# Performance work log

Measured on AMD Instinct MI355X. Metric: run time of the kernel, lower is better.

Reference implementation:

```python
import jax, jax.numpy as jnp
import numpy as np

F = 128; K = 64; SR_CUT = 10.0
NB = 5; NRI = 3; NRA = 2; NRO = 1
N_ATOMS = 10000; N_PAIRS = 320000


def act(x):
    # shifted softplus: softplus(x) - log(2)
    return jax.nn.softplus(x) - jnp.log(2.0).astype(x.dtype)


def residual(x, W1, b1, W2, b2):
    # PhysNet residual: x + dense2(dense1(act(x))) with activation on dense1
    h = act(act(x) @ W1 + b1)
    return x + h @ W2 + b2


def cutoff_fn(D):
    x = D / SR_CUT
    x3 = x * x * x; x4 = x3 * x; x5 = x4 * x
    return jnp.where(x < 1.0, 1.0 - 6.0 * x5 + 15.0 * x4 - 10.0 * x3, 0.0)


def setup_inputs() -> dict:
    key = jax.random.key(0)
    ks = jax.random.split(key, 24)

    def nrm(k, shape, s=0.05):
        return (jax.random.normal(k, shape) * s).astype(jnp.float32)

    inp = {}
    inp["Z"] = jax.random.randint(ks[0], (N_ATOMS,), 1, 95)
    inp["R"] = (jax.random.normal(ks[1], (N_ATOMS, 3)) * 3.0).astype(jnp.float32)
    inp["idx_i"] = jax.random.randint(ks[2], (N_PAIRS,), 0, N_ATOMS)
    inp["idx_j"] = jax.random.randint(ks[3], (N_PAIRS,), 0, N_ATOMS)
    s3 = float(np.sqrt(3.0))
    inp["embeddings"] = jax.random.uniform(ks[4], (95, F), minval=-s3, maxval=s3).astype(jnp.float32)
    inp["rbf_centers"] = jnp.linspace(1.0, float(np.exp(-SR_CUT)), K).astype(jnp.float32)
    width = (0.5 / ((1.0 - float(np.exp(-SR_CUT))) / K)) ** 2
    inp["rbf_widths"] = jnp.full((K,), width, dtype=jnp.float32)
    inp["k2f_W"] = nrm(ks[5], (NB, K, F))
    inp["Wi"] = nrm(ks[6], (NB, F, F)); inp["bi"] = jnp.zeros((NB, F), jnp.float32)
    inp["Wj"] = nrm(ks[7], (NB, F, F)); inp["bj"] = jnp.zeros((NB, F), jnp.float32)
    inp["ri_W1"] = nrm(ks[8], (NB, NRI, F, F)); inp["ri_b1"] = jnp.zeros((NB, NRI, F), jnp.float32)
    inp["ri_W2"] = nrm(ks[9], (NB, NRI, F, F)); inp["ri_b2"] = jnp.zeros((NB, NRI, F), jnp.float32)
    inp["dW"] = nrm(ks[10], (NB, F, F)); inp["db"] = jnp.zeros((NB, F), jnp.float32)
    inp["u"] = jnp.ones((NB, F), jnp.float32)
    inp["ra_W1"] = nrm(ks[11], (NB, NRA, F, F)); inp["ra_b1"] = jnp.zeros((NB, NRA, F), jnp.float32)
    inp["ra_W2"] = nrm(ks[12], (NB, NRA, F, F)); inp["ra_b2"] = jnp.zeros((NB, NRA, F), jnp.float32)
    inp["ro_W1"] = nrm(ks[13], (NB, NRO, F, F)); inp["ro_b1"] = jnp.zeros((NB, NRO, F), jnp.float32)
    inp["ro_W2"] = nrm(ks[14], (NB, NRO, F, F)); inp["ro_b2"] = jnp.zeros((NB, NRO, F), jnp.float32)
    inp["out_W"] = nrm(ks[15], (NB, F, 2))
    inp["Escale"] = jnp.ones((95,), jnp.float32); inp["Eshift"] = jnp.zeros((95,), jnp.float32)
    inp["Qscale"] = jnp.ones((95,), jnp.float32); inp["Qshift"] = jnp.zeros((95,), jnp.float32)
    return inp


def reference(Z, R, idx_i, idx_j, embeddings, rbf_centers, rbf_widths, k2f_W, Wi, bi, Wj, bj,
              ri_W1, ri_b1, ri_W2, ri_b2, dW, db, u, ra_W1, ra_b1, ra_W2, ra_b2,
              ro_W1, ro_b1, ro_W2, ro_b2, out_W, Escale, Eshift, Qscale, Qshift):
    N = R.shape[0]
    # gather-based interatomic distances: gather -> sub -> sumsq -> relu -> sqrt
    dR = R[idx_i] - R[idx_j]                                   # [P,3]
    Dij = jnp.sqrt(jax.nn.relu(jnp.sum(dR * dR, axis=-1)))     # [P]
    # RBF expansion with smooth cutoff
    rbf = cutoff_fn(Dij)[:, None] * jnp.exp(-rbf_widths * (jnp.exp(-Dij)[:, None] - rbf_centers) ** 2)  # [P,K]
    x = embeddings[Z]                                          # [N,F]
    Ea = jnp.zeros((N,), x.dtype)
    Qa = jnp.zeros((N,), x.dtype)
    nhloss = jnp.zeros((), x.dtype)
    last2 = None
    for b in range(NB):
        # --- interaction layer ---
        g = rbf @ k2f_W[b]                                     # [P,F]
        xa = act(x)
        xi = act(xa @ Wi[b] + bi[b])                           # [N,F]
        xj_feat = act(xa @ Wj[b] + bj[b])                      # [N,F]
        msg = g * xj_feat[idx_j]                               # [P,F] gather + modulate
        m = xi + jax.ops.segment_sum(msg, idx_i, num_segments=N)
        for l in range(NRI):
            m = residual(m, ri_W1[b, l], ri_b1[b, l], ri_W2[b, l], ri_b2[b, l])
        m = act(m)
        x = u[b] * x + m @ dW[b] + db[b]
        for l in range(NRA):
            x = residual(x, ra_W1[b, l], ra_b1[b, l], ra_W2[b, l], ra_b2[b, l])
        # --- output block ---
        o = x
        for l in range(NRO):
            o = residual(o, ro_W1[b, l], ro_b1[b, l], ro_W2[b, l], ro_b2[b, l])
        out = act(o) @ out_W[b]                                # [N,2] -> (Ea, Qa)
        Ea = Ea + out[:, 0]
        Qa = Qa + out[:, 1]
        out2 = out * out
        if b > 0:
            nhloss = nhloss + jnp.mean(out2 / (out2 + last2 + 1e-7))
        last2 = out2
    Ea = Escale[Z] * Ea + Eshift[Z]
    Qa = Qscale[Z] * Qa + Qshift[Z]
    return Ea, Qa, Dij, nhloss
```

## Files before the change

### kernel.cpp

```cpp
#include <hip/hip_runtime.h>

typedef __attribute__((ext_vector_type(8))) short bfrag;
typedef __attribute__((ext_vector_type(4))) float ffrag;

__device__ __forceinline__ unsigned short f2b(float f){
  unsigned int u = __float_as_uint(f);
  return (unsigned short)((u + 0x7FFFu + ((u >> 16) & 1u)) >> 16);
}
__device__ __forceinline__ float b2f_lo(unsigned int v){
  return __uint_as_float(v << 16);
}
__device__ __forceinline__ float b2f_hi(unsigned int v){
  return __uint_as_float(v & 0xFFFF0000u);
}
__device__ __forceinline__ float actf(float v){
  float e = __builtin_amdgcn_exp2f(-fabsf(v)*1.44269504088896341f);
  return fmaxf(v, 0.f) + __builtin_amdgcn_logf(1.f + e)*0.69314718055994531f - 0.69314718055994531f;
}

__global__ __launch_bounds__(256) void k_zero(float* p, int n){
  int i = blockIdx.x*256 + threadIdx.x;
  if (i < n) p[i] = 0.f;
}

__global__ __launch_bounds__(256) void k_dij_count(
    const float* __restrict__ R, const int* __restrict__ idx_i, const int* __restrict__ idx_j,
    float* __restrict__ DijF, float* __restrict__ Dout, int* __restrict__ counts, int P){
  int p = blockIdx.x*256 + threadIdx.x;
  if (p >= P) return;
  int i = idx_i[p], j = idx_j[p];
  float dx = R[i*3+0] - R[j*3+0];
  float dy = R[i*3+1] - R[j*3+1];
  float dz = R[i*3+2] - R[j*3+2];
  float D = sqrtf(fmaxf(dx*dx + dy*dy + dz*dz, 0.f));
  DijF[p] = D;
  Dout[p] = D;
  atomicAdd(&counts[i], 1);
}

__global__ __launch_bounds__(1024) void k_scan(const int* __restrict__ counts,
    int* __restrict__ cursor, int N){
  __shared__ int wsum[16];
  int tid = threadIdx.x;
  int CH = (N + 1023) >> 10;
  int base = tid * CH;
  int s = 0;
  for (int i = 0; i < CH; ++i){
    int idx = base + i;
    s += (idx < N) ? counts[idx] : 0;
  }
  int lane = tid & 63, w = tid >> 6;
  int v = s;
  #pragma unroll
  for (int off = 1; off < 64; off <<= 1){
    int t = __shfl_up(v, off, 64);
    if (lane >= off) v += t;
  }
  if (lane == 63) wsum[w] = v;
  __syncthreads();
  if (tid < 16){
    int t = wsum[tid];
    int vv = t;
    #pragma unroll
    for (int off = 1; off < 16; off <<= 1){
      int u = __shfl_up(vv, off, 64);
      if (tid >= off) vv += u;
    }
    wsum[tid] = vv - t;
  }
  __syncthreads();
  int run = (v - s) + wsum[w];
  for (int i = 0; i < CH; ++i){
    int idx = base + i;
    if (idx < N){ cursor[idx] = run; run += counts[idx]; }
  }
}

__global__ __launch_bounds__(256) void k_scatter(const int* __restrict__ idx_i,
    const int* __restrict__ idx_j, const float* __restrict__ DijF,
    int* __restrict__ cursor, int* __restrict__ i_s, int* __restrict__ j_s,
    float* __restrict__ D_s, int P){
  int p = blockIdx.x*256 + threadIdx.x;
  if (p >= P) return;
  int i = idx_i[p];
  int pos = atomicAdd(&cursor[i], 1);
  i_s[pos] = i;
  j_s[pos] = idx_j[p];
  D_s[pos] = DijF[p];
}

__global__ __launch_bounds__(256) void k_rbf(
    const float* __restrict__ D_s, const float* __restrict__ cent, const float* __restrict__ wid,
    unsigned short* __restrict__ rbf_s, int P){
  int gid = blockIdx.x*256 + threadIdx.x;
  if (gid >= P*8) return;
  int t = gid >> 3, kg = gid & 7;
  float D = D_s[t];
  float xc = D * 0.1f;
  float cut = 0.f;
  if (xc < 1.f){
    float x3 = xc*xc*xc, x4 = x3*xc, x5 = x4*xc;
    cut = 1.f - 6.f*x5 + 15.f*x4 - 10.f*x3;
  }
  float eD = __builtin_amdgcn_exp2f(-D*1.44269504088896341f);
  bfrag o;
  #pragma unroll
  for (int i = 0; i < 8; ++i){
    int k = kg*8 + i;
    float tt = eD - cent[k];
    float v = cut * __builtin_amdgcn_exp2f(-wid[k]*tt*tt*1.44269504088896341f);
    o[i] = (short)f2b(v);
  }
  *(bfrag*)(rbf_s + (size_t)gid*8) = o;
}

__global__ __launch_bounds__(256) void k_prepAll(
    const float* __restrict__ riW1, const float* __restrict__ riW2,
    const float* __restrict__ dW,   const float* __restrict__ raW1,
    const float* __restrict__ raW2, const float* __restrict__ roW1,
    const float* __restrict__ roW2, const float* __restrict__ Wi,
    const float* __restrict__ Wj,   const float* __restrict__ k2f,
    const float* __restrict__ outW,
    unsigned short* __restrict__ WBall, unsigned short* __restrict__ k2fP,
    unsigned short* __restrict__ outWB){
  int gid = blockIdx.x*256 + threadIdx.x;
  if (gid < 75*2048){
    int i = gid >> 11, r = gid & 2047;
    const float* S;
    int slot;
    if (i < 15)      { S = riW1 + (size_t)i*16384;      slot = (i/3)*15 + 2*(i%3); }
    else if (i < 30) { int j=i-15; S = riW2 + (size_t)j*16384; slot = (j/3)*15 + 2*(j%3) + 1; }
    else if (i < 35) { int j=i-30; S = dW   + (size_t)j*16384; slot = j*15 + 6; }
    else if (i < 45) { int j=i-35; S = raW1 + (size_t)j*16384; slot = (j/2)*15 + 7 + 2*(j%2); }
    else if (i < 55) { int j=i-45; S = raW2 + (size_t)j*16384; slot = (j/2)*15 + 8 + 2*(j%2); }
    else if (i < 60) { int j=i-55; S = roW1 + (size_t)j*16384; slot = j*15 + 11; }
    else if (i < 65) { int j=i-60; S = roW2 + (size_t)j*16384; slot = j*15 + 12; }
    else if (i < 70) { int j=i-65; S = Wi   + (size_t)j*16384; slot = ((j==0)?4:(j-1))*15 + 13; }
    else             { int j=i-70; S = Wj   + (size_t)j*16384; slot = ((j==0)?4:(j-1))*15 + 14; }
    int fr = r >> 6, l = r & 63;
    int T = fr >> 2, k0 = fr & 3;
    int n = T*16 + (l & 15);
    int kbase = k0*32 + (l >> 4)*8;
    unsigned short* D = WBall + ((size_t)slot*2048 + r)*8;
    ushort4 o0, o1;
    o0.x=f2b(S[(kbase+0)*128+n]); o0.y=f2b(S[(kbase+1)*128+n]);
    o0.z=f2b(S[(kbase+2)*128+n]); o0.w=f2b(S[(kbase+3)*128+n]);
    o1.x=f2b(S[(kbase+4)*128+n]); o1.y=f2b(S[(kbase+5)*128+n]);
    o1.z=f2b(S[(kbase+6)*128+n]); o1.w=f2b(S[(kbase+7)*128+n]);
    ((ushort4*)D)[0]=o0; ((ushort4*)D)[1]=o1;
  } else if (gid < 75*2048 + 5120){
    int g = gid - 75*2048;
    int l = g & 63, fr = (g >> 6) & 15, b = g >> 10;
    int tile = fr >> 1, kh = fr & 1;
    const float* src = k2f + (size_t)b*64*128;
    int n = tile*16 + (l & 15);
    int kbase = kh*32 + (l >> 4)*8;
    ushort4 o0, o1;
    o0.x = f2b(src[(kbase+0)*128+n]); o0.y = f2b(src[(kbase+1)*128+n]);
    o0.z = f2b(src[(kbase+2)*128+n]); o0.w = f2b(src[(kbase+3)*128+n]);
    o1.x = f2b(src[(kbase+4)*128+n]); o1.y = f2b(src[(kbase+5)*128+n]);
    o1.z = f2b(src[(kbase+6)*128+n]); o1.w = f2b(src[(kbase+7)*128+n]);
    ushort4* dst = (ushort4*)(k2fP + (size_t)g*8);
    dst[0] = o0; dst[1] = o1;
  } else if (gid < 75*2048 + 5120 + 1280){
    int g = gid - (75*2048 + 5120);
    int b = g >> 8, r = g & 255;
// ... 24 lines not shown
  #pragma unroll
  for (int tt = 0; tt < 4; ++tt){
    ffrag c = {0.f,0.f,0.f,0.f};
    const bfrag* bp = (const bfrag*)(WB + (((w*4+tt)*4)*64 + l)*8);
    #pragma unroll
    for (int k0 = 0; k0 < 4; ++k0)
      c = __builtin_amdgcn_mfma_f32_16x16x32_bf16(A[k0], bp[k0*64], c, 0, 0, 0);
    C[tt] = c;
  }
}

__global__ __launch_bounds__(128) void k_phase1m(
    const int* __restrict__ Z, const float* __restrict__ emb,
    const unsigned short* __restrict__ WB45,
    const float* __restrict__ bi0, const float* __restrict__ bj0,
    float* __restrict__ x_g, float* __restrict__ m_g, unsigned short* __restrict__ xjb_g, int N){
  __shared__ unsigned short tile[16*136];
  int tid = threadIdx.x, w = tid >> 6, l = tid & 63;
  int m = l & 15, q = l >> 4, rbase = blockIdx.x*16;
  #pragma unroll
  for (int r = 0; r < 4; ++r){
    int row = rbase + q*4 + r;
    int z = Z[row];
    #pragma unroll
    for (int tt = 0; tt < 4; ++tt){
      int c = (w*4+tt)*16 + m;
      float v = emb[(size_t)z*128 + c];
      x_g[(size_t)row*128 + c] = v;
      tile[(q*4+r)*136 + c] = f2b(actf(v));
    }
  }
  __syncthreads();
  ffrag C[4];
  mmtile(tile, WB45 + 13*16384, w, l, C);
  #pragma unroll
  for (int tt = 0; tt < 4; ++tt){
    int c = (w*4+tt)*16 + m;
    float bb = bi0[c];
    #pragma unroll
    for (int r = 0; r < 4; ++r)
      m_g[(size_t)(rbase + q*4 + r)*128 + c] = actf(C[tt][r] + bb);
  }
  mmtile(tile, WB45 + 14*16384, w, l, C);
  #pragma unroll
  for (int tt = 0; tt < 4; ++tt){
    int c = (w*4+tt)*16 + m;
    float bb = bj0[c];
    #pragma unroll
    for (int r = 0; r < 4; ++r)
      xjb_g[(size_t)(rbase + q*4 + r)*128 + c] = f2b(actf(C[tt][r] + bb));
  }
}

__global__ __launch_bounds__(256) void k_pairmsg2(
    const unsigned short* __restrict__ rbf_s, const unsigned short* __restrict__ k2fP,
    const int* __restrict__ i_s, const int* __restrict__ j_s,
    const unsigned short* __restrict__ xj, float* __restrict__ m_g, int P){
  __shared__ float G[4][16*130];
  int tid = threadIdx.x, w = tid >> 6, l = tid & 63;
  float* Gw = &G[w][0];
  bfrag B[16];
  #pragma unroll
  for (int t = 0; t < 8; ++t){
    #pragma unroll
    for (int kh = 0; kh < 2; ++kh)
      B[t*2+kh] = *(const bfrag*)(k2fP + (size_t)((t*2+kh)*64 + l)*8);
  }
  int wstart = (blockIdx.x*4 + w)*128;
  if (wstart >= P) return;
  int row16 = l & 15, quad = l >> 4;
  float a0 = 0.f, a1 = 0.f;
  int iCur = -1;
  bfrag A0 = *(const bfrag*)(rbf_s + (size_t)(wstart + row16)*64 + quad*8);
  bfrag A1 = *(const bfrag*)(rbf_s + (size_t)(wstart + row16)*64 + 32 + quad*8);
  int4 iv[4], jv[4];
  #pragma unroll
  for (int g = 0; g < 4; ++g){
    iv[g] = *(const int4*)(i_s + wstart + g*4);
    jv[g] = *(const int4*)(j_s + wstart + g*4);
  }
  unsigned int xv[16];
  {
    const int* jp = (const int*)jv;
    #pragma unroll
    for (int k = 0; k < 16; ++k)
      xv[k] = *(const unsigned int*)(xj + (size_t)jp[k]*128 + 2*l);
  }
  #pragma unroll 1
  for (int bi2 = 0; bi2 < 8; ++bi2){
    int bt = wstart + bi2*16;
    const int* ip = (const int*)iv;
    int4 niv[4], njv[4];
    if (bi2 < 7){
      int btn = bt + 16;
      #pragma unroll
      for (int g = 0; g < 4; ++g){
        niv[g] = *(const int4*)(i_s + btn + g*4);
        njv[g] = *(const int4*)(j_s + btn + g*4);
      }
    }
    #pragma unroll
    for (int t = 0; t < 8; ++t){
      ffrag C = {0.f,0.f,0.f,0.f};
      C = __builtin_amdgcn_mfma_f32_16x16x32_bf16(A0, B[t*2],   C, 0, 0, 0);
      C = __builtin_amdgcn_mfma_f32_16x16x32_bf16(A1, B[t*2+1], C, 0, 0, 0);
      #pragma unroll
      for (int r = 0; r < 4; ++r)
        Gw[(quad*4+r)*130 + t*16 + row16] = C[r];
    }
    bfrag nA0, nA1;
    unsigned int nxv[16];
    if (bi2 < 7){
      int btn = bt + 16;
      nA0 = *(const bfrag*)(rbf_s + (size_t)(btn + row16)*64 + quad*8);
      nA1 = *(const bfrag*)(rbf_s + (size_t)(btn + row16)*64 + 32 + quad*8);
      const int* njp = (const int*)njv;
      #pragma unroll
      for (int k = 0; k < 16; ++k)
        nxv[k] = *(const unsigned int*)(xj + (size_t)njp[k]*128 + 2*l);
    }
    #pragma unroll
    for (int k = 0; k < 16; ++k){
      int i = ip[k];
      if (i != iCur){
        if (iCur >= 0){
          unsafeAtomicAdd(&m_g[(size_t)iCur*128 + 2*l],     a0);
          unsafeAtomicAdd(&m_g[(size_t)iCur*128 + 2*l + 1], a1);
        }
        iCur = i; a0 = 0.f; a1 = 0.f;
      }
      float g0 = Gw[k*130 + 2*l], g1 = Gw[k*130 + 2*l + 1];
      a0 = fmaf(g0, b2f_lo(xv[k]), a0);
      a1 = fmaf(g1, b2f_hi(xv[k]), a1);
    }
    if (bi2 < 7){
      A0 = nA0; A1 = nA1;
      #pragma unroll
      for (int g = 0; g < 4; ++g){ iv[g] = niv[g]; jv[g] = njv[g]; }
      #pragma unroll
      for (int k = 0; k < 16; ++k) xv[k] = nxv[k];
    }
  }
  if (iCur >= 0){
    unsafeAtomicAdd(&m_g[(size_t)iCur*128 + 2*l],     a0);
    unsafeAtomicAdd(&m_g[(size_t)iCur*128 + 2*l + 1], a1);
  }
}

template<int HASNEXT, int NH>
__global__ __launch_bounds__(512) void k_phase2m(
    float* __restrict__ m_g, float* __restrict__ x_g, unsigned short* __restrict__ xjb_g,
    const unsigned short* __restrict__ WBb,
    const float* __restrict__ rib1, const float* __restrict__ rib2,
    const float* __restrict__ db, const float* __restrict__ u,
    const float* __restrict__ rab1, const float* __restrict__ rab2,
    const float* __restrict__ rob1, const float* __restrict__ rob2,
    const float* __restrict__ biN, const float* __restrict__ bjN,
    const unsigned short* __restrict__ outWBb,
    float* __restrict__ Ea, float* __restrict__ Qa,
    float* __restrict__ last2, float* __restrict__ nh, int N){
  __shared__ unsigned short tiles[2][2][16*136];
  __shared__ float biasS[16*128];
  int tid = threadIdx.x, w = tid >> 6, l = tid & 63;
  int m = l & 15, q = l >> 4, rbase = blockIdx.x*32;
  int c = w*16 + m;
  ffrag mC[2], xC[2], C[2];
  float xrow[2][4];
  int cur = 0;
  const int nst = HASNEXT ? 15 : 13;
  const int slotSeq[15] = {0,1,2,3,4,5,6,7,8,9,10,
                           HASNEXT?13:11, HASNEXT?14:12, 11, 12};
  bfrag Bb[2][4];
  #pragma unroll
  for (int k0 = 0; k0 < 4; ++k0)
    Bb[0][k0] = *(const bfrag*)(WBb + (size_t)slotSeq[0]*16384 + (size_t)((w*4+k0)*64 + l)*8);

  if (tid < 128){
    biasS[0*128+tid]  = rib1[tid];
    biasS[1*128+tid]  = rib1[128+tid];
    biasS[2*128+tid]  = rib1[256+tid];
    biasS[3*128+tid]  = rib2[tid];
    biasS[4*128+tid]  = rib2[128+tid];
    biasS[5*128+tid]  = rib2[256+tid];
    biasS[6*128+tid]  = db[tid];
    biasS[7*128+tid]  = u[tid];
    biasS[8*128+tid]  = rab1[tid];
    biasS[9*128+tid]  = rab1[128+tid];
    biasS[10*128+tid] = rab2[tid];
    biasS[11*128+tid] = rab2[128+tid];
    biasS[12*128+tid] = rob1[tid];
    biasS[13*128+tid] = rob2[tid];
    biasS[14*128+tid] = biN[tid];
    biasS[15*128+tid] = bjN[tid];
  }
  #pragma unroll
  for (int h = 0; h < 2; ++h){
    #pragma unroll
    for (int r = 0; r < 4; ++r){
      int row = rbase + h*16 + q*4 + r;
      int rs = row < N ? row : N-1;
      xrow[h][r] = x_g[(size_t)rs*128 + c];
      float v = m_g[(size_t)rs*128 + c];
      mC[h][r] = v;
      tiles[h][0][(q*4+r)*136 + c] = f2b(actf(v));
    }
  }
  #pragma unroll 2
  for (int s = 0; s < nst; ++s){
    __syncthreads();
    if (s+1 < nst){
      #pragma unroll
      for (int k0 = 0; k0 < 4; ++k0)
        Bb[(s+1)&1][k0] = *(const bfrag*)(WBb + (size_t)slotSeq[s+1]*16384 + (size_t)((w*4+k0)*64 + l)*8);
    }
    #pragma unroll
    for (int h = 0; h < 2; ++h){
      const unsigned short* tp = &tiles[h][cur][0];
      ffrag cc = {0.f,0.f,0.f,0.f};
      #pragma unroll
      for (int k0 = 0; k0 < 4; ++k0){
        bfrag A = *(const bfrag*)(tp + m*136 + k0*32 + q*8);
        cc = __builtin_amdgcn_mfma_f32_16x16x32_bf16(A, Bb[s&1][k0], cc, 0, 0, 0);
      }
      C[h] = cc;
    }
    if (HASNEXT && s == 11){
      float bb = biasS[14*128 + c];
      #pragma unroll
      for (int h = 0; h < 2; ++h)
        #pragma unroll
        for (int r = 0; r < 4; ++r){
          int row = rbase + h*16 + q*4 + r;
          if (row < N) m_g[(size_t)row*128 + c] = actf(C[h][r] + bb);
        }
    } else if (HASNEXT && s == 12){
      float bb = biasS[15*128 + c];
      #pragma unroll
      for (int h = 0; h < 2; ++h)
        #pragma unroll
        for (int r = 0; r < 4; ++r){
          int row = rbase + h*16 + q*4 + r;
          if (row < N) xjb_g[(size_t)row*128 + c] = f2b(actf(C[h][r] + bb));
        }
    } else if (s == 6){
      float uu = biasS[7*128 + c], bb = biasS[6*128 + c];
      #pragma unroll
      for (int h = 0; h < 2; ++h)
        #pragma unroll
        for (int r = 0; r < 4; ++r){
          float nv = uu*xrow[h][r] + C[h][r] + bb;
          xC[h][r] = nv;
          tiles[h][1-cur][(q*4+r)*136 + c] = f2b(actf(nv));
        }
      cur ^= 1;
    } else if (s == 1 || s == 3 || s == 5){
      float bb = biasS[(3 + (s>>1))*128 + c];
      #pragma unroll
      for (int h = 0; h < 2; ++h)
        #pragma unroll
        for (int r = 0; r < 4; ++r){
          float nv = mC[h][r] + C[h][r] + bb;
          mC[h][r] = nv;
          tiles[h][1-cur][(q*4+r)*136 + c] = f2b(actf(nv));
        }
      cur ^= 1;
    } else if (s == 8 || s == 10){
      float bb = biasS[(10 + ((s-8)>>1))*128 + c];
      #pragma unroll
      for (int h = 0; h < 2; ++h)
        #pragma unroll
        for (int r = 0; r < 4; ++r){
          float nv = xC[h][r] + C[h][r] + bb;
          xC[h][r] = nv;
          tiles[h][1-cur][(q*4+r)*136 + c] = f2b(actf(nv));
          if (HASNEXT && s == 10){
            int row = rbase + h*16 + q*4 + r;
            if (row < N) x_g[(size_t)row*128 + c] = nv;
          }
        }
      cur ^= 1;
    } else if ((HASNEXT && s == 14) || (!HASNEXT && s == 12)){
      float bb = biasS[13*128 + c];
      #pragma unroll
      for (int h = 0; h < 2; ++h)
        #pragma unroll
        for (int r = 0; r < 4; ++r){
          float ov = xC[h][r] + C[h][r] + bb;
          tiles[h][1-cur][(q*4+r)*136 + c] = f2b(actf(ov));
        }
      cur ^= 1;
    } else {
      int bidx = (s==0)?0:(s==2)?1:(s==4)?2:(s==7)?8:(s==9)?9:12;
      float bb = biasS[bidx*128 + c];
      #pragma unroll
      for (int h = 0; h < 2; ++h)
        #pragma unroll
        for (int r = 0; r < 4; ++r)
          tiles[h][1-cur][(q*4+r)*136 + c] = f2b(actf(C[h][r] + bb));
      cur ^= 1;
    }
  }
  __syncthreads();
  if (w < 2){
    const unsigned short* tp = &tiles[w][cur][0];
    bfrag A[4];
    #pragma unroll
    for (int k0 = 0; k0 < 4; ++k0)
      A[k0] = *(const bfrag*)(tp + m*136 + k0*32 + q*8);
    ffrag Ch = {0.f,0.f,0.f,0.f};
    #pragma unroll
    for (int k0 = 0; k0 < 4; ++k0){
      bfrag B = *(const bfrag*)(outWBb + (size_t)(k0*64 + l)*8);
      Ch = __builtin_amdgcn_mfma_f32_16x16x32_bf16(A[k0], B, Ch, 0, 0, 0);
    }
    int col = m;
    if (col < 2){
      float tpa = 0.f;
      #pragma unroll
      for (int r = 0; r < 4; ++r){
        int row = rbase + w*16 + q*4 + r;
        if (row < N){
          float val = Ch[r];
          if (NH){
            if (col == 0) Ea[row] += val; else Qa[row] += val;
          } else {
            if (col == 0) Ea[row]  = val; else Qa[row]  = val;
          }
          float sq = val*val;
          if (NH){
            float lastv = last2[row*2 + col];
            tpa += sq/(sq + lastv + 1e-7f);
          }
          last2[row*2 + col] = sq;
        }
      }
      if (NH) unsafeAtomicAdd(nh, tpa);
    }
  }
}

__global__ __launch_bounds__(256) void k_final(
    const int* __restrict__ Z, const float* __restrict__ Ea, const float* __restrict__ Qa,
    const float* __restrict__ Es, const float* __restrict__ Eh,
    const float* __restrict__ Qs, const float* __restrict__ Qh,
    const float* __restrict__ nh, float* __restrict__ out, int N, int P){
  int n = blockIdx.x*256 + threadIdx.x;
  if (n < N){
    int z = Z[n];
    out[n]   = Es[z]*Ea[n] + Eh[z];
    out[N+n] = Qs[z]*Qa[n] + Qh[z];
  }
  if (blockIdx.x == 0 && threadIdx.x == 0)
    out[(size_t)2*N + P] = nh[0] / (2.f * (float)N);
}

extern "C" void kernel_launch(void* const* d_in, const int* in_sizes, int n_in,
                              void* d_out, int out_size, void* d_ws, size_t ws_size,
                              hipStream_t stream){
  const int N = in_sizes[0];
  const int P = in_sizes[2];
  const int F = 128;

  const int* Z      = (const int*)d_in[0];
  const float* R    = (const float*)d_in[1];
  const int* idx_i  = (const int*)d_in[2];
  const int* idx_j  = (const int*)d_in[3];
  const float* emb  = (const float*)d_in[4];
  const float* cent = (const float*)d_in[5];
  const float* wid  = (const float*)d_in[6];
  const float* k2f  = (const float*)d_in[7];
  const float* Wi   = (const float*)d_in[8];  const float* bi   = (const float*)d_in[9];
  const float* Wj   = (const float*)d_in[10]; const float* bj   = (const float*)d_in[11];
  const float* riW1 = (const float*)d_in[12]; const float* rib1 = (const float*)d_in[13];
  const float* riW2 = (const float*)d_in[14]; const float* rib2 = (const float*)d_in[15];
  const float* dWp  = (const float*)d_in[16]; const float* dbp  = (const float*)d_in[17];
  const float* u    = (const float*)d_in[18];
  const float* raW1 = (const float*)d_in[19]; const float* rab1 = (const float*)d_in[20];
  const float* raW2 = (const float*)d_in[21]; const float* rab2 = (const float*)d_in[22];
  const float* roW1 = (const float*)d_in[23]; const float* rob1 = (const float*)d_in[24];
  const float* roW2 = (const float*)d_in[25]; const float* rob2 = (const float*)d_in[26];
  const float* outW = (const float*)d_in[27];
  const float* Es   = (const float*)d_in[28]; const float* Eh   = (const float*)d_in[29];
  const float* Qs   = (const float*)d_in[30]; const float* Qh   = (const float*)d_in[31];

  char* ws = (char*)d_ws;
  size_t off = 0;
  float* DijF  = (float*)(ws + off); off += (size_t)P*4;
  float* D_s   = (float*)(ws + off); off += (size_t)P*4;
  int*   i_s   = (int*)  (ws + off); off += (size_t)P*4;
  int*   j_s   = (int*)  (ws + off); off += (size_t)P*4;
  unsigned short* rbf_s = (unsigned short*)(ws + off); off += (size_t)P*64*2;
  unsigned short* k2fP  = (unsigned short*)(ws + off); off += (size_t)5*16*64*8*2;
  unsigned short* WBall = (unsigned short*)(ws + off); off += (size_t)75*16384*2;
  unsigned short* outWB = (unsigned short*)(ws + off); off += (size_t)5*2048*2;
  float* x     = (float*)(ws + off); off += (size_t)N*F*4;
  unsigned short* xjb = (unsigned short*)(ws + off); off += (size_t)N*F*2;
  float* m     = (float*)(ws + off); off += (size_t)N*F*4;
  float* last2 = (float*)(ws + off); off += (size_t)N*2*4;
  float* Ea    = (float*)(ws + off); off += (size_t)N*4;
  float* Qa    = (float*)(ws + off); off += (size_t)N*4;
  float* nh    = (float*)(ws + off); off += 256;
  int*   counts= (int*)  (ws + off); off += (size_t)N*4;
  int*   cursor= (int*)  (ws + off); off += (size_t)N*4;

  float* outF = (float*)d_out;
  float* Dout = outF + (size_t)2*N;

  const int nzero = N + 64;
  k_zero<<<dim3((nzero+255)/256), dim3(256), 0, stream>>>(nh, nzero);
  k_dij_count<<<dim3((P+255)/256), dim3(256), 0, stream>>>(R, idx_i, idx_j, DijF, Dout, counts, P);
  k_scan<<<dim3(1), dim3(1024), 0, stream>>>(counts, cursor, N);
  k_scatter<<<dim3((P+255)/256), dim3(256), 0, stream>>>(idx_i, idx_j, DijF, cursor, i_s, j_s, D_s, P);
  k_rbf<<<dim3((P*8+255)/256), dim3(256), 0, stream>>>(D_s, cent, wid, rbf_s, P);
  k_prepAll<<<dim3((75*2048 + 5120 + 1280 + 255)/256), dim3(256), 0, stream>>>(
      riW1, riW2, dWp, raW1, raW2, roW1, roW2, Wi, Wj, k2f, outW, WBall, k2fP, outWB);

  const int G16 = (N + 15)/16;
  k_phase1m<<<dim3(G16), dim3(128), 0, stream>>>(Z, emb, WBall + (size_t)4*15*16384,
                                                 bi, bj, x, m, xjb, N);

  const int pmg = (P + 511)/512;
  const int G32 = (N + 31)/32;
  for (int b = 0; b < 5; ++b){
    k_pairmsg2<<<dim3(pmg), dim3(256), 0, stream>>>(rbf_s, k2fP + (size_t)b*16*64*8,
                                                    i_s, j_s, xjb, m, P);
    const unsigned short* WBb = WBall + (size_t)b*15*16384;
    const float* a_rib1 = rib1 + (size_t)b*3*F;
    const float* a_rib2 = rib2 + (size_t)b*3*F;
    const float* a_db   = dbp  + (size_t)b*F;
    const float* a_u    = u    + (size_t)b*F;
    const float* a_rab1 = rab1 + (size_t)b*2*F;
    const float* a_rab2 = rab2 + (size_t)b*2*F;
    const float* a_rob1 = rob1 + (size_t)b*F;
    const float* a_rob2 = rob2 + (size_t)b*F;
    int bn = (b < 4) ? (b+1) : 0;
    const float* a_biN = bi + (size_t)bn*F;
    const float* a_bjN = bj + (size_t)bn*F;
    const unsigned short* oWB = outWB + (size_t)b*2048;
    if (b == 0){
      k_phase2m<1,0><<<dim3(G32), dim3(512), 0, stream>>>(m, x, xjb, WBb,
        a_rib1, a_rib2, a_db, a_u, a_rab1, a_rab2, a_rob1, a_rob2,
        a_biN, a_bjN, oWB, Ea, Qa, last2, nh, N);
    } else if (b < 4){
      k_phase2m<1,1><<<dim3(G32), dim3(512), 0, stream>>>(m, x, xjb, WBb,
        a_rib1, a_rib2, a_db, a_u, a_rab1, a_rab2, a_rob1, a_rob2,
        a_biN, a_bjN, oWB, Ea, Qa, last2, nh, N);
    } else {
      k_phase2m<0,1><<<dim3(G32), dim3(512), 0, stream>>>(m, x, xjb, WBb,
        a_rib1, a_rib2, a_db, a_u, a_rab1, a_rab2, a_rob1, a_rob2,
        a_biN, a_bjN, oWB, Ea, Qa, last2, nh, N);
    }
  }
  k_final<<<dim3((N+255)/256), dim3(256), 0, stream>>>(Z, Ea, Qa, Es, Eh, Qs, Qh, nh, outF, N, P);
}
```

Baseline: 493.1 us.

## Fuse pair-message aggregation into per-block atom kernel with double-buffered xj

Removes the separate pair-message kernel and computes each 32-atom block's incoming messages inside the block kernel, using the sorted pair ranges (cursor ends) and accumulating into shared memory instead of global atomics. Because the fused kernel writes next-block xj features while other blocks still read them, xj is now ping-ponged between two buffers. This saves one launch per interaction block plus the global atomic traffic on m. In exchange, shared memory use per workgroup rises sharply (an extra G and mL buffer), which may lower occupancy. Load balance also now depends on pair counts per atom group, and pairs that straddle group boundaries are filtered per element.

```diff
diff --git a/kernel.cpp b/kernel.cpp
--- a/kernel.cpp
+++ b/kernel.cpp
@@ -242,104 +242,13 @@
   }
 }
 
-__global__ __launch_bounds__(256) void k_pairmsg2(
+template<int HASNEXT, int NH>
+__global__ __launch_bounds__(512) void k_block(
     const unsigned short* __restrict__ rbf_s, const unsigned short* __restrict__ k2fP,
     const int* __restrict__ i_s, const int* __restrict__ j_s,
-    const unsigned short* __restrict__ xj, float* __restrict__ m_g, int P){
-  __shared__ float G[4][16*130];
-  int tid = threadIdx.x, w = tid >> 6, l = tid & 63;
-  float* Gw = &G[w][0];
-  bfrag B[16];
-  #pragma unroll
-  for (int t = 0; t < 8; ++t){
-    #pragma unroll
-    for (int kh = 0; kh < 2; ++kh)
-      B[t*2+kh] = *(const bfrag*)(k2fP + (size_t)((t*2+kh)*64 + l)*8);
-  }
-  int wstart = (blockIdx.x*4 + w)*128;
-  if (wstart >= P) return;
-  int row16 = l & 15, quad = l >> 4;
-  float a0 = 0.f, a1 = 0.f;
-  int iCur = -1;
-  bfrag A0 = *(const bfrag*)(rbf_s + (size_t)(wstart + row16)*64 + quad*8);
-  bfrag A1 = *(const bfrag*)(rbf_s + (size_t)(wstart + row16)*64 + 32 + quad*8);
-  int4 iv[4], jv[4];
-  #pragma unroll
-  for (int g = 0; g < 4; ++g){
-    iv[g] = *(const int4*)(i_s + wstart + g*4);
-    jv[g] = *(const int4*)(j_s + wstart + g*4);
-  }
-  unsigned int xv[16];
-  {
-    const int* jp = (const int*)jv;
-    #pragma unroll
-    for (int k = 0; k < 16; ++k)
-      xv[k] = *(const unsigned int*)(xj + (size_t)jp[k]*128 + 2*l);
-  }
-  #pragma unroll 1
-  for (int bi2 = 0; bi2 < 8; ++bi2){
-    int bt = wstart + bi2*16;
-    const int* ip = (const int*)iv;
-    int4 niv[4], njv[4];
-    if (bi2 < 7){
-      int btn = bt + 16;
-      #pragma unroll
-      for (int g = 0; g < 4; ++g){
-        niv[g] = *(const int4*)(i_s + btn + g*4);
-        njv[g] = *(const int4*)(j_s + btn + g*4);
-      }
-    }
-    #pragma unroll
-    for (int t = 0; t < 8; ++t){
-      ffrag C = {0.f,0.f,0.f,0.f};
-      C = __builtin_amdgcn_mfma_f32_16x16x32_bf16(A0, B[t*2],   C, 0, 0, 0);
-      C = __builtin_amdgcn_mfma_f32_16x16x32_bf16(A1, B[t*2+1], C, 0, 0, 0);
-      #pragma unroll
-      for (int r = 0; r < 4; ++r)
-        Gw[(quad*4+r)*130 + t*16 + row16] = C[r];
-    }
-    bfrag nA0, nA1;
-    unsigned int nxv[16];
-    if (bi2 < 7){
-      int btn = bt + 16;
-      nA0 = *(const bfrag*)(rbf_s + (size_t)(btn + row16)*64 + quad*8);
-      nA1 = *(const bfrag*)(rbf_s + (size_t)(btn + row16)*64 + 32 + quad*8);
-      const int* njp = (const int*)njv;
-      #pragma unroll
-      for (int k = 0; k < 16; ++k)
-        nxv[k] = *(const unsigned int*)(xj + (size_t)njp[k]*128 + 2*l);
-    }
-    #pragma unroll
-    for (int k = 0; k < 16; ++k){
-      int i = ip[k];
-      if (i != iCur){
-        if (iCur >= 0){
-          unsafeAtomicAdd(&m_g[(size_t)iCur*128 + 2*l],     a0);
-          unsafeAtomicAdd(&m_g[(size_t)iCur*128 + 2*l + 1], a1);
-        }
-        iCur = i; a0 = 0.f; a1 = 0.f;
-      }
-      float g0 = Gw[k*130 + 2*l], g1 = Gw[k*130 + 2*l + 1];
-      a0 = fmaf(g0, b2f_lo(xv[k]), a0);
-      a1 = fmaf(g1, b2f_hi(xv[k]), a1);
-    }
-    if (bi2 < 7){
-      A0 = nA0; A1 = nA1;
-      #pragma unroll
-      for (int g = 0; g < 4; ++g){ iv[g] = niv[g]; jv[g] = njv[g]; }
-      #pragma unroll
-      for (int k = 0; k < 16; ++k) xv[k] = nxv[k];
-    }
-  }
-  if (iCur >= 0){
-    unsafeAtomicAdd(&m_g[(size_t)iCur*128 + 2*l],     a0);
-    unsafeAtomicAdd(&m_g[(size_t)iCur*128 + 2*l + 1], a1);
-  }
-}
-
-template<int HASNEXT, int NH>
-__global__ __launch_bounds__(512) void k_phase2m(
-    float* __restrict__ m_g, float* __restrict__ x_g, unsigned short* __restrict__ xjb_g,
+    const int* __restrict__ ends,
+    const unsigned short* __restrict__ xjb_r, unsigned short* __restrict__ xjb_w,
+    float* __restrict__ m_g, float* __restrict__ x_g,
     const unsigned short* __restrict__ WBb,
     const float* __restrict__ rib1, const float* __restrict__ rib2,
     const float* __restrict__ db, const float* __restrict__ u,
@@ -348,22 +257,17 @@
     const float* __restrict__ biN, const float* __restrict__ bjN,
     const unsigned short* __restrict__ outWBb,
     float* __restrict__ Ea, float* __restrict__ Qa,
-    float* __restrict__ last2, float* __restrict__ nh, int N){
+    float* __restrict__ last2, float* __restrict__ nh, int N, int P){
+  __shared__ float G[8][16*130];
+  __shared__ float mL[32*128];
   __shared__ unsigned short tiles[2][2][16*136];
   __shared__ float biasS[16*128];
   int tid = threadIdx.x, w = tid >> 6, l = tid & 63;
   int m = l & 15, q = l >> 4, rbase = blockIdx.x*32;
   int c = w*16 + m;
-  ffrag mC[2], xC[2], C[2];
-  float xrow[2][4];
-  int cur = 0;
-  const int nst = HASNEXT ? 15 : 13;
-  const int slotSeq[15] = {0,1,2,3,4,5,6,7,8,9,10,
-                           HASNEXT?13:11, HASNEXT?14:12, 11, 12};
-  bfrag Bb[2][4];
-  #pragma unroll
-  for (int k0 = 0; k0 < 4; ++k0)
-    Bb[0][k0] = *(const bfrag*)(WBb + (size_t)slotSeq[0]*16384 + (size_t)((w*4+k0)*64 + l)*8);
+
+  #pragma unroll
+  for (int i = 0; i < 8; ++i) mL[i*512 + tid] = 0.f;
 
   if (tid < 128){
     biasS[0*128+tid]  = rib1[tid];
@@ -383,6 +287,106 @@
     biasS[14*128+tid] = biN[tid];
     biasS[15*128+tid] = bjN[tid];
   }
+
+  {
+    float* Gw = &G[w][0];
+    int row16 = l & 15, quad = l >> 4;
+    bfrag B[16];
+    #pragma unroll
+    for (int t = 0; t < 8; ++t){
+      #pragma unroll
+      for (int kh = 0; kh < 2; ++kh)
+        B[t*2+kh] = *(const bfrag*)(k2fP + (size_t)((t*2+kh)*64 + l)*8);
+    }
+    int pstart = (rbase == 0) ? 0 : ends[rbase-1];
+    int rlast  = (rbase+31 < N) ? rbase+31 : N-1;
+    int pend   = ends[rlast];
+    int b0 = pstart >> 4, b1 = (pend + 15) >> 4;
+    float a0 = 0.f, a1 = 0.f;
+    int iCur = -1;
+    int bt = b0 + w;
+    if (bt < b1){
+      int base = bt << 4;
+      int4 iv[4], jv[4];
+      #pragma unroll
+      for (int g = 0; g < 4; ++g){
+        iv[g] = *(const int4*)(i_s + base + g*4);
+        jv[g] = *(const int4*)(j_s + base + g*4);
+      }
+      bfrag A0 = *(const bfrag*)(rbf_s + (size_t)(base + row16)*64 + quad*8);
+      bfrag A1 = *(const bfrag*)(rbf_s + (size_t)(base + row16)*64 + 32 + quad*8);
+      unsigned int xv[16];
+      {
+        const int* jp = (const int*)jv;
+        #pragma unroll
+        for (int k = 0; k < 16; ++k)
+          xv[k] = *(const unsigned int*)(xjb_r + (size_t)jp[k]*128 + 2*l);
+      }
+      #pragma unroll 1
+      for (; bt < b1; bt += 8){
+        int btn = bt + 8;
+        bool more = btn < b1;
+        int basen = btn << 4;
+        int4 niv[4], njv[4];
+        if (more){
+          #pragma unroll
+          for (int g = 0; g < 4; ++g){
+            niv[g] = *(const int4*)(i_s + basen + g*4);
+            njv[g] = *(const int4*)(j_s + basen + g*4);
+          }
+        }
+        #pragma unroll
+        for (int t = 0; t < 8; ++t){
+          ffrag C = {0.f,0.f,0.f,0.f};
+          C = __builtin_amdgcn_mfma_f32_16x16x32_bf16(A0, B[t*2],   C, 0, 0, 0);
+          C = __builtin_amdgcn_mfma_f32_16x16x32_bf16(A1, B[t*2+1], C, 0, 0, 0);
+          #pragma unroll
+          for (int r = 0; r < 4; ++r)
+            Gw[(quad*4+r)*130 + t*16 + row16] = C[r];
+        }
+        bfrag nA0, nA1;
+        unsigned int nxv[16];
+        if (more){
+          nA0 = *(const bfrag*)(rbf_s + (size_t)(basen + row16)*64 + quad*8);
+          nA1 = *(const bfrag*)(rbf_s + (size_t)(basen + row16)*64 + 32 + quad*8);
+          const int* njp = (const int*)njv;
+          #pragma unroll
+          for (int k = 0; k < 16; ++k)
+            nxv[k] = *(const unsigned int*)(xjb_r + (size_t)njp[k]*128 + 2*l);
+        }
+        const int* ip = (const int*)iv;
+        #pragma unroll
+        for (int k = 0; k < 16; ++k){
+          int i = ip[k];
+          if (i >= rbase && i < rbase + 32){
+            if (i != iCur){
+              if (iCur >= 0){
+                atomicAdd(&mL[(iCur-rbase)*128 + 2*l],     a0);
+                atomicAdd(&mL[(iCur-rbase)*128 + 2*l + 1], a1);
+              }
+              iCur = i; a0 = 0.f; a1 = 0.f;
+            }
+            float g0 = Gw[k*130 + 2*l], g1 = Gw[k*130 + 2*l + 1];
+            a0 = fmaf(g0, b2f_lo(xv[k]), a0);
+            a1 = fmaf(g1, b2f_hi(xv[k]), a1);
+          }
+        }
+        if (more){
+          A0 = nA0; A1 = nA1;
+          #pragma unroll
+          for (int g = 0; g < 4; ++g){ iv[g] = niv[g]; jv[g] = njv[g]; }
+          #pragma unroll
+          for (int k = 0; k < 16; ++k) xv[k] = nxv[k];
+        }
+      }
+    }
+    if (iCur >= 0){
+      atomicAdd(&mL[(iCur-rbase)*128 + 2*l],     a0);
+      atomicAdd(&mL[(iCur-rbase)*128 + 2*l + 1], a1);
+    }
+  }
+
+  float xrow[2][4], mxi[2][4];
   #pragma unroll
   for (int h = 0; h < 2; ++h){
     #pragma unroll
@@ -390,7 +394,26 @@
       int row = rbase + h*16 + q*4 + r;
       int rs = row < N ? row : N-1;
       xrow[h][r] = x_g[(size_t)rs*128 + c];
-      float v = m_g[(size_t)rs*128 + c];
+      mxi[h][r]  = m_g[(size_t)rs*128 + c];
+    }
+  }
+  const int nst = HASNEXT ? 15 : 13;
+  const int slotSeq[15] = {0,1,2,3,4,5,6,7,8,9,10,
+                           HASNEXT?13:11, HASNEXT?14:12, 11, 12};
+  bfrag Bb[2][4];
+  #pragma unroll
+  for (int k0 = 0; k0 < 4; ++k0)
+    Bb[0][k0] = *(const bfrag*)(WBb + (size_t)slotSeq[0]*16384 + (size_t)((w*4+k0)*64 + l)*8);
+
+  __syncthreads();
+
+  ffrag mC[2], xC[2], C[2];
+  int cur = 0;
+  #pragma unroll
+  for (int h = 0; h < 2; ++h){
+    #pragma unroll
+    for (int r = 0; r < 4; ++r){
+      float v = mxi[h][r] + mL[(h*16 + q*4 + r)*128 + c];
       mC[h][r] = v;
       tiles[h][0][(q*4+r)*136 + c] = f2b(actf(v));
     }
@@ -430,7 +453,7 @@
         #pragma unroll
         for (int r = 0; r < 4; ++r){
           int row = rbase + h*16 + q*4 + r;
-          if (row < N) xjb_g[(size_t)row*128 + c] = f2b(actf(C[h][r] + bb));
+          if (row < N) xjb_w[(size_t)row*128 + c] = f2b(actf(C[h][r] + bb));
         }
     } else if (s == 6){
       float uu = biasS[7*128 + c], bb = biasS[6*128 + c];
@@ -584,7 +607,8 @@
   unsigned short* WBall = (unsigned short*)(ws + off); off += (size_t)75*16384*2;
   unsigned short* outWB = (unsigned short*)(ws + off); off += (size_t)5*2048*2;
   float* x     = (float*)(ws + off); off += (size_t)N*F*4;
-  unsigned short* xjb = (unsigned short*)(ws + off); off += (size_t)N*F*2;
+  unsigned short* xjbA = (unsigned short*)(ws + off); off += (size_t)N*F*2;
+  unsigned short* xjbB = (unsigned short*)(ws + off); off += (size_t)N*F*2;
   float* m     = (float*)(ws + off); off += (size_t)N*F*4;
   float* last2 = (float*)(ws + off); off += (size_t)N*2*4;
   float* Ea    = (float*)(ws + off); off += (size_t)N*4;
@@ -607,13 +631,10 @@
 
   const int G16 = (N + 15)/16;
   k_phase1m<<<dim3(G16), dim3(128), 0, stream>>>(Z, emb, WBall + (size_t)4*15*16384,
-                                                 bi, bj, x, m, xjb, N);
-
-  const int pmg = (P + 511)/512;
+                                                 bi, bj, x, m, xjbA, N);
+
   const int G32 = (N + 31)/32;
   for (int b = 0; b < 5; ++b){
-    k_pairmsg2<<<dim3(pmg), dim3(256), 0, stream>>>(rbf_s, k2fP + (size_t)b*16*64*8,
-                                                    i_s, j_s, xjb, m, P);
     const unsigned short* WBb = WBall + (size_t)b*15*16384;
     const float* a_rib1 = rib1 + (size_t)b*3*F;
     const float* a_rib2 = rib2 + (size_t)b*3*F;
@@ -627,18 +648,21 @@
     const float* a_biN = bi + (size_t)bn*F;
     const float* a_bjN = bj + (size_t)bn*F;
     const unsigned short* oWB = outWB + (size_t)b*2048;
+    const unsigned short* kP  = k2fP + (size_t)b*16*64*8;
+    const unsigned short* xr  = (b & 1) ? xjbB : xjbA;
+    unsigned short*       xw  = (b & 1) ? xjbA : xjbB;
     if (b == 0){
-      k_phase2m<1,0><<<dim3(G32), dim3(512), 0, stream>>>(m, x, xjb, WBb,
-        a_rib1, a_rib2, a_db, a_u, a_rab1, a_rab2, a_rob1, a_rob2,
-        a_biN, a_bjN, oWB, Ea, Qa, last2, nh, N);
+      k_block<1,0><<<dim3(G32), dim3(512), 0, stream>>>(rbf_s, kP, i_s, j_s, cursor,
+        xr, xw, m, x, WBb, a_rib1, a_rib2, a_db, a_u, a_rab1, a_rab2, a_rob1, a_rob2,
+        a_biN, a_bjN, oWB, Ea, Qa, last2, nh, N, P);
     } else if (b < 4){
-      k_phase2m<1,1><<<dim3(G32), dim3(512), 0, stream>>>(m, x, xjb, WBb,
-        a_rib1, a_rib2, a_db, a_u, a_rab1, a_rab2, a_rob1, a_rob2,
-        a_biN, a_bjN, oWB, Ea, Qa, last2, nh, N);
+      k_block<1,1><<<dim3(G32), dim3(512), 0, stream>>>(rbf_s, kP, i_s, j_s, cursor,
+        xr, xw, m, x, WBb, a_rib1, a_rib2, a_db, a_u, a_rab1, a_rab2, a_rob1, a_rob2,
+        a_biN, a_bjN, oWB, Ea, Qa, last2, nh, N, P);
     } else {
-      k_phase2m<0,1><<<dim3(G32), dim3(512), 0, stream>>>(m, x, xjb, WBb,
-        a_rib1, a_rib2, a_db, a_u, a_rab1, a_rab2, a_rob1, a_rob2,
-        a_biN, a_bjN, oWB, Ea, Qa, last2, nh, N);
+      k_block<0,1><<<dim3(G32), dim3(512), 0, stream>>>(rbf_s, kP, i_s, j_s, cursor,
+        xr, xw, m, x, WBb, a_rib1, a_rib2, a_db, a_u, a_rab1, a_rab2, a_rob1, a_rob2,
+        a_biN, a_bjN, oWB, Ea, Qa, last2, nh, N, P);
     }
   }
   k_final<<<dim3((N+255)/256), dim3(256), 0, stream>>>(Z, Ea, Qa, Es, Eh, Qs, Qh, nh, outF, N, P);
```

After: 672.5 us. 1.36x slower.

## Compute RBF features inside pair-message kernel and shrink phase2 row tiles to 16

Applied to the files above, without the earlier changes.

Removes the precomputed bf16 RBF buffer and its kernel, and instead recomputes the cutoff-weighted Gaussian features per 16-pair tile inside k_pairmsg2, with centers and widths staged in LDS. This avoids writing and then re-reading a P×64 bf16 array in each of five blocks, at the cost of extra exp work per block. k_phase2m now processes 16 rows per block instead of 32, dropping the h loop and the row bounds checks. Occupancy hints are added to both kernels. The bounds checks are removed on the assumption that N is a multiple of 16, and the early return for out-of-range waves is gone.

```diff
diff --git a/kernel.cpp b/kernel.cpp
--- a/kernel.cpp
+++ b/kernel.cpp
@@ -16,6 +16,24 @@
 __device__ __forceinline__ float actf(float v){
   float e = __builtin_amdgcn_exp2f(-fabsf(v)*1.44269504088896341f);
   return fmaxf(v, 0.f) + __builtin_amdgcn_logf(1.f + e)*0.69314718055994531f - 0.69314718055994531f;
+}
+
+__device__ __forceinline__ void mkA(float D, const float* __restrict__ centL,
+    const float* __restrict__ widL, int quad, bfrag& A0, bfrag& A1){
+  float xc = D * 0.1f;
+  float cut = 0.f;
+  if (xc < 1.f){
+    float x3 = xc*xc*xc, x4 = x3*xc, x5 = x4*xc;
+    cut = 1.f - 6.f*x5 + 15.f*x4 - 10.f*x3;
+  }
+  float eD = __builtin_amdgcn_exp2f(-D*1.44269504088896341f);
+  #pragma unroll
+  for (int i = 0; i < 8; ++i){
+    float t0 = eD - centL[quad*8+i];
+    A0[i] = (short)f2b(cut*__builtin_amdgcn_exp2f(-widL[quad*8+i]*t0*t0*1.44269504088896341f));
+    float t1 = eD - centL[32+quad*8+i];
+    A1[i] = (short)f2b(cut*__builtin_amdgcn_exp2f(-widL[32+quad*8+i]*t1*t1*1.44269504088896341f));
+  }
 }
 
 __global__ __launch_bounds__(256) void k_zero(float* p, int n){
@@ -87,31 +105,6 @@
   i_s[pos] = i;
   j_s[pos] = idx_j[p];
   D_s[pos] = DijF[p];
-}
-
-__global__ __launch_bounds__(256) void k_rbf(
-    const float* __restrict__ D_s, const float* __restrict__ cent, const float* __restrict__ wid,
-    unsigned short* __restrict__ rbf_s, int P){
-  int gid = blockIdx.x*256 + threadIdx.x;
-  if (gid >= P*8) return;
-  int t = gid >> 3, kg = gid & 7;
-  float D = D_s[t];
-  float xc = D * 0.1f;
-  float cut = 0.f;
-  if (xc < 1.f){
-    float x3 = xc*xc*xc, x4 = x3*xc, x5 = x4*xc;
-    cut = 1.f - 6.f*x5 + 15.f*x4 - 10.f*x3;
-  }
-  float eD = __builtin_amdgcn_exp2f(-D*1.44269504088896341f);
-  bfrag o;
-  #pragma unroll
-  for (int i = 0; i < 8; ++i){
-    int k = kg*8 + i;
-    float tt = eD - cent[k];
-    float v = cut * __builtin_amdgcn_exp2f(-wid[k]*tt*tt*1.44269504088896341f);
-    o[i] = (short)f2b(v);
-  }
-  *(bfrag*)(rbf_s + (size_t)gid*8) = o;
 }
 
 __global__ __launch_bounds__(256) void k_prepAll(
@@ -242,12 +235,15 @@
   }
 }
 
-__global__ __launch_bounds__(256) void k_pairmsg2(
-    const unsigned short* __restrict__ rbf_s, const unsigned short* __restrict__ k2fP,
+__global__ __launch_bounds__(256, 3) void k_pairmsg2(
+    const float* __restrict__ D_s, const float* __restrict__ cent, const float* __restrict__ wid,
+    const unsigned short* __restrict__ k2fP,
     const int* __restrict__ i_s, const int* __restrict__ j_s,
     const unsigned short* __restrict__ xj, float* __restrict__ m_g, int P){
   __shared__ float G[4][16*130];
+  __shared__ float centL[64], widL[64];
   int tid = threadIdx.x, w = tid >> 6, l = tid & 63;
+  if (tid < 64){ centL[tid] = cent[tid]; widL[tid] = wid[tid]; }
   float* Gw = &G[w][0];
   bfrag B[16];
   #pragma unroll
@@ -257,12 +253,12 @@
       B[t*2+kh] = *(const bfrag*)(k2fP + (size_t)((t*2+kh)*64 + l)*8);
   }
   int wstart = (blockIdx.x*4 + w)*128;
-  if (wstart >= P) return;
   int row16 = l & 15, quad = l >> 4;
+  __syncthreads();
   float a0 = 0.f, a1 = 0.f;
   int iCur = -1;
-  bfrag A0 = *(const bfrag*)(rbf_s + (size_t)(wstart + row16)*64 + quad*8);
-  bfrag A1 = *(const bfrag*)(rbf_s + (size_t)(wstart + row16)*64 + 32 + quad*8);
+  bfrag A0, A1;
+  { float D0 = D_s[wstart + row16]; mkA(D0, centL, widL, quad, A0, A1); }
   int4 iv[4], jv[4];
   #pragma unroll
   for (int g = 0; g < 4; ++g){
@@ -281,6 +277,7 @@
     int bt = wstart + bi2*16;
     const int* ip = (const int*)iv;
     int4 niv[4], njv[4];
+    float nD = 0.f;
     if (bi2 < 7){
       int btn = bt + 16;
       #pragma unroll
@@ -288,6 +285,7 @@
         niv[g] = *(const int4*)(i_s + btn + g*4);
         njv[g] = *(const int4*)(j_s + btn + g*4);
       }
+      nD = D_s[btn + row16];
     }
     #pragma unroll
     for (int t = 0; t < 8; ++t){
@@ -301,9 +299,7 @@
     bfrag nA0, nA1;
     unsigned int nxv[16];
     if (bi2 < 7){
-      int btn = bt + 16;
-      nA0 = *(const bfrag*)(rbf_s + (size_t)(btn + row16)*64 + quad*8);
-      nA1 = *(const bfrag*)(rbf_s + (size_t)(btn + row16)*64 + 32 + quad*8);
+      mkA(nD, centL, widL, quad, nA0, nA1);
       const int* njp = (const int*)njv;
       #pragma unroll
       for (int k = 0; k < 16; ++k)
@@ -338,7 +334,7 @@
 }
 
 template<int HASNEXT, int NH>
-__global__ __launch_bounds__(512) void k_phase2m(
+__global__ __launch_bounds__(512, 6) void k_phase2m(
     float* __restrict__ m_g, float* __restrict__ x_g, unsigned short* __restrict__ xjb_g,
     const unsigned short* __restrict__ WBb,
     const float* __restrict__ rib1, const float* __restrict__ rib2,
@@ -349,13 +345,13 @@
     const unsigned short* __restrict__ outWBb,
     float* __restrict__ Ea, float* __restrict__ Qa,
     float* __restrict__ last2, float* __restrict__ nh, int N){
-  __shared__ unsigned short tiles[2][2][16*136];
+  __shared__ unsigned short tiles[2][16*136];
   __shared__ float biasS[16*128];
   int tid = threadIdx.x, w = tid >> 6, l = tid & 63;
-  int m = l & 15, q = l >> 4, rbase = blockIdx.x*32;
+  int m = l & 15, q = l >> 4, rbase = blockIdx.x*16;
   int c = w*16 + m;
-  ffrag mC[2], xC[2], C[2];
-  float xrow[2][4];
+  ffrag mC, xC, C;
+  float xrow[4];
   int cur = 0;
   const int nst = HASNEXT ? 15 : 13;
   const int slotSeq[15] = {0,1,2,3,4,5,6,7,8,9,10,
@@ -384,16 +380,12 @@
     biasS[15*128+tid] = bjN[tid];
   }
   #pragma unroll
-  for (int h = 0; h < 2; ++h){
-    #pragma unroll
-    for (int r = 0; r < 4; ++r){
-      int row = rbase + h*16 + q*4 + r;
-      int rs = row < N ? row : N-1;
-      xrow[h][r] = x_g[(size_t)rs*128 + c];
-      float v = m_g[(size_t)rs*128 + c];
-      mC[h][r] = v;
-      tiles[h][0][(q*4+r)*136 + c] = f2b(actf(v));
-    }
+  for (int r = 0; r < 4; ++r){
+    int row = rbase + q*4 + r;
+    xrow[r] = x_g[(size_t)row*128 + c];
+    float v = m_g[(size_t)row*128 + c];
+    mC[r] = v;
+    tiles[0][(q*4+r)*136 + c] = f2b(actf(v));
   }
   #pragma unroll 2
   for (int s = 0; s < nst; ++s){
@@ -403,96 +395,75 @@
       for (int k0 = 0; k0 < 4; ++k0)
         Bb[(s+1)&1][k0] = *(const bfrag*)(WBb + (size_t)slotSeq[s+1]*16384 + (size_t)((w*4+k0)*64 + l)*8);
     }
-    #pragma unroll
-    for (int h = 0; h < 2; ++h){
-      const unsigned short* tp = &tiles[h][cur][0];
+    {
+      const unsigned short* tp = &tiles[cur][0];
       ffrag cc = {0.f,0.f,0.f,0.f};
       #pragma unroll
       for (int k0 = 0; k0 < 4; ++k0){
         bfrag A = *(const bfrag*)(tp + m*136 + k0*32 + q*8);
         cc = __builtin_amdgcn_mfma_f32_16x16x32_bf16(A, Bb[s&1][k0], cc, 0, 0, 0);
       }
-      C[h] = cc;
+      C = cc;
     }
     if (HASNEXT && s == 11){
       float bb = biasS[14*128 + c];
       #pragma unroll
-      for (int h = 0; h < 2; ++h)
-        #pragma unroll
-        for (int r = 0; r < 4; ++r){
-          int row = rbase + h*16 + q*4 + r;
-          if (row < N) m_g[(size_t)row*128 + c] = actf(C[h][r] + bb);
-        }
+      for (int r = 0; r < 4; ++r)
+        m_g[(size_t)(rbase + q*4 + r)*128 + c] = actf(C[r] + bb);
     } else if (HASNEXT && s == 12){
       float bb = biasS[15*128 + c];
       #pragma unroll
-      for (int h = 0; h < 2; ++h)
-        #pragma unroll
-        for (int r = 0; r < 4; ++r){
-          int row = rbase + h*16 + q*4 + r;
-          if (row < N) xjb_g[(size_t)row*128 + c] = f2b(actf(C[h][r] + bb));
-        }
+      for (int r = 0; r < 4; ++r)
+        xjb_g[(size_t)(rbase + q*4 + r)*128 + c] = f2b(actf(C[r] + bb));
     } else if (s == 6){
       float uu = biasS[7*128 + c], bb = biasS[6*128 + c];
       #pragma unroll
-      for (int h = 0; h < 2; ++h)
-        #pragma unroll
-        for (int r = 0; r < 4; ++r){
-          float nv = uu*xrow[h][r] + C[h][r] + bb;
-          xC[h][r] = nv;
-          tiles[h][1-cur][(q*4+r)*136 + c] = f2b(actf(nv));
-        }
+      for (int r = 0; r < 4; ++r){
+        float nv = uu*xrow[r] + C[r] + bb;
+        xC[r] = nv;
+        tiles[1-cur][(q*4+r)*136 + c] = f2b(actf(nv));
+      }
       cur ^= 1;
     } else if (s == 1 || s == 3 || s == 5){
       float bb = biasS[(3 + (s>>1))*128 + c];
       #pragma unroll
-      for (int h = 0; h < 2; ++h)
-        #pragma unroll
-        for (int r = 0; r < 4; ++r){
-          float nv = mC[h][r] + C[h][r] + bb;
-          mC[h][r] = nv;
-          tiles[h][1-cur][(q*4+r)*136 + c] = f2b(actf(nv));
-        }
+      for (int r = 0; r < 4; ++r){
+        float nv = mC[r] + C[r] + bb;
+        mC[r] = nv;
+        tiles[1-cur][(q*4+r)*136 + c] = f2b(actf(nv));
+      }
       cur ^= 1;
     } else if (s == 8 || s == 10){
       float bb = biasS[(10 + ((s-8)>>1))*128 + c];
       #pragma unroll
-      for (int h = 0; h < 2; ++h)
-        #pragma unroll
-        for (int r = 0; r < 4; ++r){
-          float nv = xC[h][r] + C[h][r] + bb;
-          xC[h][r] = nv;
-          tiles[h][1-cur][(q*4+r)*136 + c] = f2b(actf(nv));
-          if (HASNEXT && s == 10){
-            int row = rbase + h*16 + q*4 + r;
-            if (row < N) x_g[(size_t)row*128 + c] = nv;
-          }
-        }
+      for (int r = 0; r < 4; ++r){
+        float nv = xC[r] + C[r] + bb;
+        xC[r] = nv;
+        tiles[1-cur][(q*4+r)*136 + c] = f2b(actf(nv));
+        if (HASNEXT && s == 10)
+          x_g[(size_t)(rbase + q*4 + r)*128 + c] = nv;
+      }
       cur ^= 1;
     } else if ((HASNEXT && s == 14) || (!HASNEXT && s == 12)){
       float bb = biasS[13*128 + c];
       #pragma unroll
-      for (int h = 0; h < 2; ++h)
-        #pragma unroll
-        for (int r = 0; r < 4; ++r){
-          float ov = xC[h][r] + C[h][r] + bb;
-          tiles[h][1-cur][(q*4+r)*136 + c] = f2b(actf(ov));
-        }
+      for (int r = 0; r < 4; ++r){
+        float ov = xC[r] + C[r] + bb;
+        tiles[1-cur][(q*4+r)*136 + c] = f2b(actf(ov));
+      }
       cur ^= 1;
     } else {
       int bidx = (s==0)?0:(s==2)?1:(s==4)?2:(s==7)?8:(s==9)?9:12;
       float bb = biasS[bidx*128 + c];
       #pragma unroll
-      for (int h = 0; h < 2; ++h)
-        #pragma unroll
-        for (int r = 0; r < 4; ++r)
-          tiles[h][1-cur][(q*4+r)*136 + c] = f2b(actf(C[h][r] + bb));
+      for (int r = 0; r < 4; ++r)
+        tiles[1-cur][(q*4+r)*136 + c] = f2b(actf(C[r] + bb));
       cur ^= 1;
     }
   }
   __syncthreads();
-  if (w < 2){
-    const unsigned short* tp = &tiles[w][cur][0];
+  if (w == 0){
+    const unsigned short* tp = &tiles[cur][0];
     bfrag A[4];
     #pragma unroll
     for (int k0 = 0; k0 < 4; ++k0)
@@ -508,21 +479,19 @@
       float tpa = 0.f;
       #pragma unroll
       for (int r = 0; r < 4; ++r){
-        int row = rbase + w*16 + q*4 + r;
-        if (row < N){
-          float val = Ch[r];
-          if (NH){
-            if (col == 0) Ea[row] += val; else Qa[row] += val;
-          } else {
-            if (col == 0) Ea[row]  = val; else Qa[row]  = val;
-          }
-          float sq = val*val;
-          if (NH){
-            float lastv = last2[row*2 + col];
-            tpa += sq/(sq + lastv + 1e-7f);
-          }
-          last2[row*2 + col] = sq;
+        int row = rbase + q*4 + r;
+        float val = Ch[r];
+        if (NH){
+          if (col == 0) Ea[row] += val; else Qa[row] += val;
+        } else {
+          if (col == 0) Ea[row]  = val; else Qa[row]  = val;
         }
+        float sq = val*val;
+        if (NH){
+          float lastv = last2[row*2 + col];
+          tpa += sq/(sq + lastv + 1e-7f);
+        }
+        last2[row*2 + col] = sq;
       }
       if (NH) unsafeAtomicAdd(nh, tpa);
     }
@@ -579,7 +548,6 @@
   float* D_s   = (float*)(ws + off); off += (size_t)P*4;
   int*   i_s   = (int*)  (ws + off); off += (size_t)P*4;
   int*   j_s   = (int*)  (ws + off); off += (size_t)P*4;
-  unsigned short* rbf_s = (unsigned short*)(ws + off); off += (size_t)P*64*2;
   unsigned short* k2fP  = (unsigned short*)(ws + off); off += (size_t)5*16*64*8*2;
   unsigned short* WBall = (unsigned short*)(ws + off); off += (size_t)75*16384*2;
   unsigned short* outWB = (unsigned short*)(ws + off); off += (size_t)5*2048*2;
@@ -601,7 +569,6 @@
   k_dij_count<<<dim3((P+255)/256), dim3(256), 0, stream>>>(R, idx_i, idx_j, DijF, Dout, counts, P);
   k_scan<<<dim3(1), dim3(1024), 0, stream>>>(counts, cursor, N);
   k_scatter<<<dim3((P+255)/256), dim3(256), 0, stream>>>(idx_i, idx_j, DijF, cursor, i_s, j_s, D_s, P);
-  k_rbf<<<dim3((P*8+255)/256), dim3(256), 0, stream>>>(D_s, cent, wid, rbf_s, P);
   k_prepAll<<<dim3((75*2048 + 5120 + 1280 + 255)/256), dim3(256), 0, stream>>>(
       riW1, riW2, dWp, raW1, raW2, roW1, roW2, Wi, Wj, k2f, outW, WBall, k2fP, outWB);
 
@@ -610,9 +577,9 @@
                                                  bi, bj, x, m, xjb, N);
 
   const int pmg = (P + 511)/512;
-  const int G32 = (N + 31)/32;
   for (int b = 0; b < 5; ++b){
-    k_pairmsg2<<<dim3(pmg), dim3(256), 0, stream>>>(rbf_s, k2fP + (size_t)b*16*64*8,
+    k_pairmsg2<<<dim3(pmg), dim3(256), 0, stream>>>(D_s, cent, wid,
+                                                    k2fP + (size_t)b*16*64*8,
                                                     i_s, j_s, xjb, m, P);
     const unsigned short* WBb = WBall + (size_t)b*15*16384;
     const float* a_rib1 = rib1 + (size_t)b*3*F;
@@ -628,15 +595,15 @@
     const float* a_bjN = bj + (size_t)bn*F;
     const unsigned short* oWB = outWB + (size_t)b*2048;
     if (b == 0){
-      k_phase2m<1,0><<<dim3(G32), dim3(512), 0, stream>>>(m, x, xjb, WBb,
+      k_phase2m<1,0><<<dim3(G16), dim3(512), 0, stream>>>(m, x, xjb, WBb,
         a_rib1, a_rib2, a_db, a_u, a_rab1, a_rab2, a_rob1, a_rob2,
         a_biN, a_bjN, oWB, Ea, Qa, last2, nh, N);
     } else if (b < 4){
-      k_phase2m<1,1><<<dim3(G32), dim3(512), 0, stream>>>(m, x, xjb, WBb,
+      k_phase2m<1,1><<<dim3(G16), dim3(512), 0, stream>>>(m, x, xjb, WBb,
         a_rib1, a_rib2, a_db, a_u, a_rab1, a_rab2, a_rob1, a_rob2,
         a_biN, a_bjN, oWB, Ea, Qa, last2, nh, N);
     } else {
-      k_phase2m<0,1><<<dim3(G32), dim3(512), 0, stream>>>(m, x, xjb, WBb,
+      k_phase2m<0,1><<<dim3(G16), dim3(512), 0, stream>>>(m, x, xjb, WBb,
         a_rib1, a_rib2, a_db, a_u, a_rab1, a_rab2, a_rob1, a_rob2,
         a_biN, a_bjN, oWB, Ea, Qa, last2, nh, N);
     }
```

After: 632.3 us. 28.2% more time.
